# Kernel tuning notes

Measured on AMD Instinct MI355X. Metric: run time of the kernel, lower is better.

Reference implementation:

```python
import jax, jax.numpy as jnp
import numpy as np

B, L, D_MODEL = 2, 1024, 1024
N_LAYERS = 2
D_INNER = 2 * D_MODEL          # expand = 2
D_STATE = 16
D_CONV = 4
DT_RANK = (D_MODEL + 15) // 16  # ceil(d_model/16) = 64
INIT_SCALE = 0.02


def setup_inputs() -> dict:
    key = jax.random.key(0)
    ks = jax.random.split(key, 8)
    f32 = jnp.float32
    dt_init = float(np.log(np.expm1(0.01)))  # softplus^-1(0.01), standard mamba dt bias init
    return {
        "x": jax.random.normal(ks[0], (B, L, D_MODEL), f32),
        "W_in": jax.random.normal(ks[1], (N_LAYERS, 2 * D_INNER, D_MODEL), f32) * INIT_SCALE,
        "conv_w": jax.random.normal(ks[2], (N_LAYERS, D_INNER, D_CONV), f32) * INIT_SCALE,
        "conv_b": jnp.zeros((N_LAYERS, D_INNER), f32),
        "W_x": jax.random.normal(ks[3], (N_LAYERS, DT_RANK + 2 * D_STATE, D_INNER), f32) * INIT_SCALE,
        "W_dt": jax.random.normal(ks[4], (N_LAYERS, D_INNER, DT_RANK), f32) * INIT_SCALE,
        "b_dt": jnp.full((N_LAYERS, D_INNER), dt_init, f32),
        "A_log": jnp.tile(jnp.log(jnp.arange(1, D_STATE + 1, dtype=f32)), (N_LAYERS, D_INNER, 1)),
        "D": jnp.ones((N_LAYERS, D_INNER), f32),
        "W_out": jax.random.normal(ks[5], (N_LAYERS, D_MODEL, D_INNER), f32) * INIT_SCALE,
    }


def _silu(x):
    return x * jax.nn.sigmoid(x)


def _causal_conv1d(u, w, b):
    # u: [B, L, D_INNER], w: [D_INNER, D_CONV] depthwise, b: [D_INNER]
    ut = jnp.pad(jnp.transpose(u, (0, 2, 1)), ((0, 0), (0, 0), (D_CONV - 1, 0)))
    y = jax.lax.conv_general_dilated(
        ut, w[:, None, :], window_strides=(1,), padding='VALID',
        feature_group_count=D_INNER, dimension_numbers=('NCH', 'OIH', 'NCH'))
    return jnp.transpose(y + b[None, :, None], (0, 2, 1))


def _selective_scan(u, dt, A, Bm, Cm, Dvec):
    # u, dt: [B, L, D_INNER]; A: [D_INNER, N]; Bm, Cm: [B, L, N]; Dvec: [D_INNER]
    dA = jnp.exp(dt[..., None] * A)                        # [B,L,Din,N]
    dBu = dt[..., None] * Bm[:, :, None, :] * u[..., None]  # [B,L,Din,N]

    def step(h, xs):
        dA_t, dBu_t, C_t = xs                              # [B,Din,N],[B,Din,N],[B,N]
        h = dA_t * h + dBu_t
        y = jnp.einsum('bdn,bn->bd', h, C_t)
        return h, y

    h0 = jnp.zeros((u.shape[0], D_INNER, D_STATE), u.dtype)
    _, ys = jax.lax.scan(step, h0, (jnp.swapaxes(dA, 0, 1),
                                    jnp.swapaxes(dBu, 0, 1),
                                    jnp.swapaxes(Cm, 0, 1)))
    return jnp.swapaxes(ys, 0, 1) + u * Dvec               # [B,L,Din]


def _mamba_layer(x, W_in, conv_w, conv_b, W_x, W_dt, b_dt, A_log, Dvec, W_out):
    xz = jnp.einsum('bld,ed->ble', x, W_in)                # [B,L,2*Din]
    u, z = jnp.split(xz, 2, axis=-1)
    u = _silu(_causal_conv1d(u, conv_w, conv_b))
    x_dbl = jnp.einsum('bld,rd->blr', u, W_x)              # [B,L,dt_rank+2N]
    dt, Bm, Cm = jnp.split(x_dbl, [DT_RANK, DT_RANK + D_STATE], axis=-1)
    dt = jax.nn.softplus(jnp.einsum('blr,dr->bld', dt, W_dt) + b_dt)
    A = -jnp.exp(A_log)
    y = _selective_scan(u, dt, A, Bm, Cm, Dvec)
    y = y * _silu(z)
    return jnp.einsum('bld,od->blo', y, W_out)


def reference(x, W_in, conv_w, conv_b, W_x, W_dt, b_dt, A_log, D, W_out):
    residual = x
    h = x
    for i in range(N_LAYERS):
        h = _mamba_layer(h, W_in[i], conv_w[i], conv_b[i], W_x[i],
                         W_dt[i], b_dt[i], A_log[i], D[i], W_out[i])
    return h + residual
```

## Files before the change

### kernel.cpp

```cpp
#include <hip/hip_runtime.h>
#include <hip/hip_bf16.h>
#include <math.h>

#define B_ 2
#define L_ 1024
#define DM 1024
#define DIN 2048
#define DS 16
#define DTR 64
#define CHL 32
#define NCH 32

typedef __attribute__((ext_vector_type(8))) short bf16x8;
typedef __attribute__((ext_vector_type(8))) unsigned short u16x8;
typedef __attribute__((ext_vector_type(4))) unsigned short u16x4;
typedef __attribute__((ext_vector_type(4))) float f32x4;
typedef unsigned short ushort_t;
typedef unsigned int uint_t;

__device__ __forceinline__ float sigmoidf_(float x) { return 1.f / (1.f + __expf(-x)); }
__device__ __forceinline__ ushort_t f2b(float f) {
    uint_t b = __float_as_uint(f);
    return (ushort_t)((b + 0x7FFFu + ((b >> 16) & 1u)) >> 16);
}
__device__ __forceinline__ float b2f(ushort_t u) {
    return __uint_as_float(((uint_t)u) << 16);
}

__global__ __launch_bounds__(256) void f2b_all_k(
    const float* __restrict__ s0, ushort_t* __restrict__ d0, int n0,
    const float* __restrict__ s1, ushort_t* __restrict__ d1, int n1,
    const float* __restrict__ s2, ushort_t* __restrict__ d2, int n2,
    const float* __restrict__ s3, ushort_t* __restrict__ d3, int n3,
    const float* __restrict__ s4, ushort_t* __restrict__ d4, int n4)
{
    int i = (blockIdx.x * 256 + threadIdx.x) * 4;
    const float* s; ushort_t* d;
    if (i < n0) { s = s0; d = d0; }
    else { i -= n0;
    if (i < n1) { s = s1; d = d1; }
    else { i -= n1;
    if (i < n2) { s = s2; d = d2; }
    else { i -= n2;
    if (i < n3) { s = s3; d = d3; }
    else { i -= n3;
    if (i < n4) { s = s4; d = d4; }
    else return; }}}}
    float4 v = *(const float4*)(s + i);
    u16x4 o;
    o[0] = f2b(v.x); o[1] = f2b(v.y); o[2] = f2b(v.z); o[3] = f2b(v.w);
    *(u16x4*)(d + i) = o;
}

__device__ __forceinline__ int xcd_swz(int wgid, int nwg) {
    int cpx = nwg >> 3;
    return (wgid & 7) * cpx + (wgid >> 3);
}

__global__ __launch_bounds__(512) void mgemm_w(const ushort_t* __restrict__ A,
    const ushort_t* __restrict__ Bt, ushort_t* __restrict__ Cb,
    int M, int N, int K, int lda, int ldb)
{
    __shared__ ushort_t sA[2][128 * 32];
    __shared__ ushort_t sB[2][256 * 32];
    const int tid = threadIdx.x;
    const int lane = tid & 63, wv = tid >> 6;
    const int wm = wv >> 2, wn = wv & 3;
    const int swz = xcd_swz(blockIdx.y * gridDim.x + blockIdx.x, gridDim.x * gridDim.y);
    const int m0 = (swz / gridDim.x) * 128, n0 = (swz % gridDim.x) * 256;
    const int sr = tid >> 2;
    const int sc = (tid & 3) * 8;
    f32x4 acc[4][4] = {};

    __builtin_amdgcn_global_load_lds(
        (const uint_t*)(A + (size_t)(m0 + sr) * lda + sc),
        (uint_t*)(sA[0] + sr * 32 + sc), 16, 0, 0);
#pragma unroll
    for (int it = 0; it < 2; ++it) {
        int rb = (tid + it * 512) >> 2;
        __builtin_amdgcn_global_load_lds(
            (const uint_t*)(Bt + (size_t)(n0 + rb) * ldb + sc),
            (uint_t*)(sB[0] + rb * 32 + sc), 16, 0, 0);
    }
    __syncthreads();
    int cur = 0;
    for (int k0 = 0; k0 < K; k0 += 32) {
        if (k0 + 32 < K) {
            int nxt = cur ^ 1;
            __builtin_amdgcn_global_load_lds(
                (const uint_t*)(A + (size_t)(m0 + sr) * lda + k0 + 32 + sc),
                (uint_t*)(sA[nxt] + sr * 32 + sc), 16, 0, 0);
#pragma unroll
            for (int it = 0; it < 2; ++it) {
                int rb = (tid + it * 512) >> 2;
                __builtin_amdgcn_global_load_lds(
                    (const uint_t*)(Bt + (size_t)(n0 + rb) * ldb + k0 + 32 + sc),
                    (uint_t*)(sB[nxt] + rb * 32 + sc), 16, 0, 0);
            }
        }
        bf16x8 af[4], bfr[4];
#pragma unroll
        for (int i = 0; i < 4; ++i) {
            af[i]  = *(const bf16x8*)(sA[cur] + (wm * 64 + i * 16 + (lane & 15)) * 32 + (lane >> 4) * 8);
            bfr[i] = *(const bf16x8*)(sB[cur] + (wn * 64 + i * 16 + (lane & 15)) * 32 + (lane >> 4) * 8);
        }
#pragma unroll
        for (int i = 0; i < 4; ++i)
#pragma unroll
            for (int jj = 0; jj < 4; ++jj)
                acc[i][jj] = __builtin_amdgcn_mfma_f32_16x16x32_bf16(af[i], bfr[jj], acc[i][jj], 0, 0, 0);
        __syncthreads();
        cur ^= 1;
    }

    const int cr = (lane >> 4) * 4, cc = lane & 15;
#pragma unroll
    for (int i = 0; i < 4; ++i) {
        int mrow = m0 + wm * 64 + i * 16 + cr;
#pragma unroll
        for (int jj = 0; jj < 4; ++jj) {
            int ncol = n0 + wn * 64 + jj * 16 + cc;
#pragma unroll
            for (int r = 0; r < 4; ++r)
                Cb[(size_t)(mrow + r) * N + ncol] = f2b(acc[i][jj][r]);
        }
    }
}

__global__ __launch_bounds__(256) void mgemm_dt(const ushort_t* __restrict__ A,
    const ushort_t* __restrict__ Bt, ushort_t* __restrict__ Cb,
    const float* __restrict__ bias, int M, int N, int K, int lda, int ldb)
{
    __shared__ ushort_t sA[2][128 * 32];
    __shared__ ushort_t sB[2][128 * 32];
    const int tid = threadIdx.x;
    const int lane = tid & 63, wv = tid >> 6;
    const int wm = wv >> 1, wn = wv & 1;
    const int swz = xcd_swz(blockIdx.y * gridDim.x + blockIdx.x, gridDim.x * gridDim.y);
    const int m0 = (swz / gridDim.x) * 128, n0 = (swz % gridDim.x) * 128;
    const int sr = tid >> 2;
    const int sc = (tid & 3) * 8;
    f32x4 acc[4][4] = {};

#pragma unroll
    for (int j = 0; j < 2; ++j) {
        int ra = sr + j * 64;
        __builtin_amdgcn_global_load_lds(
            (const uint_t*)(A + (size_t)(m0 + ra) * lda + sc),
            (uint_t*)(sA[0] + ra * 32 + sc), 16, 0, 0);
        int gb = n0 + ra; if (gb >= N) gb = N - 1;
        __builtin_amdgcn_global_load_lds(
            (const uint_t*)(Bt + (size_t)gb * ldb + sc),
            (uint_t*)(sB[0] + ra * 32 + sc), 16, 0, 0);
    }
    __syncthreads();
    int cur = 0;
    for (int k0 = 0; k0 < K; k0 += 32) {
        if (k0 + 32 < K) {
            int nxt = cur ^ 1;
#pragma unroll
            for (int j = 0; j < 2; ++j) {
                int ra = sr + j * 64;
                __builtin_amdgcn_global_load_lds(
                    (const uint_t*)(A + (size_t)(m0 + ra) * lda + k0 + 32 + sc),
                    (uint_t*)(sA[nxt] + ra * 32 + sc), 16, 0, 0);
                int gb = n0 + ra; if (gb >= N) gb = N - 1;
                __builtin_amdgcn_global_load_lds(
                    (const uint_t*)(Bt + (size_t)gb * ldb + k0 + 32 + sc),
                    (uint_t*)(sB[nxt] + ra * 32 + sc), 16, 0, 0);
            }
        }
        bf16x8 af[4], bfr[4];
#pragma unroll
        for (int i = 0; i < 4; ++i) {
            af[i]  = *(const bf16x8*)(sA[cur] + (wm * 64 + i * 16 + (lane & 15)) * 32 + (lane >> 4) * 8);
            bfr[i] = *(const bf16x8*)(sB[cur] + (wn * 64 + i * 16 + (lane & 15)) * 32 + (lane >> 4) * 8);
        }
#pragma unroll
        for (int i = 0; i < 4; ++i)
#pragma unroll
            for (int jj = 0; jj < 4; ++jj)
                acc[i][jj] = __builtin_amdgcn_mfma_f32_16x16x32_bf16(af[i], bfr[jj], acc[i][jj], 0, 0, 0);
        __syncthreads();
        cur ^= 1;
    }

    const int cr = (lane >> 4) * 4, cc = lane & 15;
#pragma unroll
    for (int i = 0; i < 4; ++i) {
        int mrow = m0 + wm * 64 + i * 16 + cr;
#pragma unroll
        for (int jj = 0; jj < 4; ++jj) {
            int ncol = n0 + wn * 64 + jj * 16 + cc;
            if (ncol < N) {
#pragma unroll
                for (int r = 0; r < 4; ++r) {
                    float v = acc[i][jj][r];
                    size_t off = (size_t)(mrow + r) * N + ncol;
                    float s = v + bias[ncol];
                    Cb[off] = f2b((s > 20.f) ? s : log1pf(expf(s)));
                }
            }
        }
    }
}

__global__ __launch_bounds__(256) void mgemm_sk(const ushort_t* __restrict__ A,
    const ushort_t* __restrict__ Bt, float* __restrict__ P,
    int M, int N, int Kslice, int lda, int ldb)
{
    __shared__ ushort_t sA[2][128 * 32];
    __shared__ ushort_t sB[2][128 * 32];
    const int tid = threadIdx.x;
    const int lane = tid & 63, wv = tid >> 6;
    const int wm = wv >> 1, wn = wv & 1;
    const int m0 = blockIdx.y * 128;
    const int kbase = blockIdx.z * Kslice;
    const int sr = tid >> 2;
    const int sc = (tid & 3) * 8;
    f32x4 acc[4][4] = {};

#pragma unroll
    for (int j = 0; j < 2; ++j) {
        int ra = sr + j * 64;
        __builtin_amdgcn_global_load_lds(
            (const uint_t*)(A + (size_t)(m0 + ra) * lda + kbase + sc),
            (uint_t*)(sA[0] + ra * 32 + sc), 16, 0, 0);
        int gb = ra; if (gb >= N) gb = N - 1;
        __builtin_amdgcn_global_load_lds(
            (const uint_t*)(Bt + (size_t)gb * ldb + kbase + sc),
            (uint_t*)(sB[0] + ra * 32 + sc), 16, 0, 0);
    }
    __syncthreads();
    int cur = 0;
    for (int k0 = kbase; k0 < kbase + Kslice; k0 += 32) {
        if (k0 + 32 < kbase + Kslice) {
            int nxt = cur ^ 1;
#pragma unroll
            for (int j = 0; j < 2; ++j) {
                int ra = sr + j * 64;
                __builtin_amdgcn_global_load_lds(
                    (const uint_t*)(A + (size_t)(m0 + ra) * lda + k0 + 32 + sc),
                    (uint_t*)(sA[nxt] + ra * 32 + sc), 16, 0, 0);
                int gb = ra; if (gb >= N) gb = N - 1;
                __builtin_amdgcn_global_load_lds(
                    (const uint_t*)(Bt + (size_t)gb * ldb + k0 + 32 + sc),
                    (uint_t*)(sB[nxt] + ra * 32 + sc), 16, 0, 0);
            }
        }
        bf16x8 af[4], bfr[4];
#pragma unroll
        for (int i = 0; i < 4; ++i) {
            af[i]  = *(const bf16x8*)(sA[cur] + (wm * 64 + i * 16 + (lane & 15)) * 32 + (lane >> 4) * 8);
            bfr[i] = *(const bf16x8*)(sB[cur] + (wn * 64 + i * 16 + (lane & 15)) * 32 + (lane >> 4) * 8);
        }
#pragma unroll
        for (int i = 0; i < 4; ++i)
#pragma unroll
            for (int jj = 0; jj < 4; ++jj)
                acc[i][jj] = __builtin_amdgcn_mfma_f32_16x16x32_bf16(af[i], bfr[jj], acc[i][jj], 0, 0, 0);
        __syncthreads();
        cur ^= 1;
    }

    const int cr = (lane >> 4) * 4, cc = lane & 15;
    float* Pz = P + (size_t)blockIdx.z * M * 96;
#pragma unroll
    for (int i = 0; i < 4; ++i) {
        int mrow = m0 + wm * 64 + i * 16 + cr;
#pragma unroll
        for (int jj = 0; jj < 4; ++jj) {
            int ncol = wn * 64 + jj * 16 + cc;
            if (ncol < 96) {
#pragma unroll
                for (int r = 0; r < 4; ++r)
                    Pz[(size_t)(mrow + r) * 96 + ncol] = acc[i][jj][r];
            }
        }
    }
}

__global__ __launch_bounds__(256) void wxred_k(const float* __restrict__ P,
    float* __restrict__ xdbl, ushort_t* __restrict__ xdblb)
{
    int idx = blockIdx.x * 256 + threadIdx.x;
    float s = 0.f;
#pragma unroll
    for (int z = 0; z < 8; ++z) s += P[(size_t)z * 196608 + idx];
    xdbl[idx] = s;
    xdblb[idx] = f2b(s);
}

template<int EPI>
__global__ __launch_bounds__(256) void mgemm_n64(const ushort_t* __restrict__ A,
    const ushort_t* __restrict__ Bt, float* __restrict__ Cf, ushort_t* __restrict__ Cb,
    const float* __restrict__ res, int M, int N, int K, int lda, int ldb)
{
    __shared__ ushort_t sA[2][128 * 32];
    __shared__ ushort_t sB[2][64 * 32];
    const int tid = threadIdx.x;
    const int lane = tid & 63, wv = tid >> 6;
    const int swz = xcd_swz(blockIdx.y * gridDim.x + blockIdx.x, gridDim.x * gridDim.y);
    const int m0 = (swz / gridDim.x) * 128, n0 = (swz % gridDim.x) * 64;
    const int sr = tid >> 2;
    const int sc = (tid & 3) * 8;
    f32x4 acc[2][4] = {};

#pragma unroll
    for (int j = 0; j < 2; ++j) {
        int ra = sr + j * 64;
        __builtin_amdgcn_global_load_lds(
            (const uint_t*)(A + (size_t)(m0 + ra) * lda + sc),
            (uint_t*)(sA[0] + ra * 32 + sc), 16, 0, 0);
    }
    __builtin_amdgcn_global_load_lds(
        (const uint_t*)(Bt + (size_t)(n0 + sr) * ldb + sc),
        (uint_t*)(sB[0] + sr * 32 + sc), 16, 0, 0);
    __syncthreads();
    int cur = 0;
    for (int k0 = 0; k0 < K; k0 += 32) {
        if (k0 + 32 < K) {
            int nxt = cur ^ 1;
#pragma unroll
            for (int j = 0; j < 2; ++j) {
                int ra = sr + j * 64;
                __builtin_amdgcn_global_load_lds(
                    (const uint_t*)(A + (size_t)(m0 + ra) * lda + k0 + 32 + sc),
                    (uint_t*)(sA[nxt] + ra * 32 + sc), 16, 0, 0);
            }
            __builtin_amdgcn_global_load_lds(
                (const uint_t*)(Bt + (size_t)(n0 + sr) * ldb + k0 + 32 + sc),
                (uint_t*)(sB[nxt] + sr * 32 + sc), 16, 0, 0);
        }
        bf16x8 af[2], bfr[4];
#pragma unroll
        for (int i = 0; i < 2; ++i)
            af[i]  = *(const bf16x8*)(sA[cur] + (wv * 32 + i * 16 + (lane & 15)) * 32 + (lane >> 4) * 8);
#pragma unroll
        for (int jj = 0; jj < 4; ++jj)
            bfr[jj] = *(const bf16x8*)(sB[cur] + (jj * 16 + (lane & 15)) * 32 + (lane >> 4) * 8);
#pragma unroll
        for (int i = 0; i < 2; ++i)
#pragma unroll
            for (int jj = 0; jj < 4; ++jj)
                acc[i][jj] = __builtin_amdgcn_mfma_f32_16x16x32_bf16(af[i], bfr[jj], acc[i][jj], 0, 0, 0);
        __syncthreads();
        cur ^= 1;
    }

    const int cr = (lane >> 4) * 4, cc = lane & 15;
#pragma unroll
    for (int i = 0; i < 2; ++i) {
        int mrow = m0 + wv * 32 + i * 16 + cr;
#pragma unroll
        for (int jj = 0; jj < 4; ++jj) {
            int ncol = n0 + jj * 16 + cc;
#pragma unroll
            for (int r = 0; r < 4; ++r) {
                float v = acc[i][jj][r];
                size_t off = (size_t)(mrow + r) * N + ncol;
                if (EPI == 3) Cb[off] = f2b(v);
                else Cf[off] = v + res[off];
            }
        }
    }
}

__global__ __launch_bounds__(256) void conv8_k(const ushort_t* __restrict__ xzb,
    const float* __restrict__ cw, const float* __restrict__ cb,
    ushort_t* __restrict__ ucb)
{
    int idx8 = blockIdx.x * 256 + threadIdx.x;
    int d8 = (idx8 & 255) * 8;
    int t = (idx8 >> 8) & (L_ - 1);
    int b = idx8 >> 18;
    const ushort_t* base = xzb + (size_t)b * L_ * (2 * DIN) + d8;
    float acc[8];
    const float4* cb4 = (const float4*)(cb + d8);
    float4 cbl = cb4[0], cbh = cb4[1];
#pragma unroll
    for (int e = 0; e < 4; ++e) { acc[e] = ((const float*)&cbl)[e]; acc[4 + e] = ((const float*)&cbh)[e]; }
    float4 cwv[8];
#pragma unroll
    for (int e = 0; e < 8; ++e) cwv[e] = ((const float4*)cw)[d8 + e];
#pragma unroll
    for (int j = 0; j < 4; ++j) {
        int tt = t - 3 + j;
        if (tt >= 0) {
            u16x8 row = *(const u16x8*)(base + (size_t)tt * (2 * DIN));
#pragma unroll
            for (int e = 0; e < 8; ++e)
                acc[e] = fmaf(((const float*)&cwv[e])[j], b2f(row[e]), acc[e]);
        }
    }
    u16x8 ob;
#pragma unroll
    for (int e = 0; e < 8; ++e) {
        float v = acc[e] * sigmoidf_(acc[e]);
        ob[e] = f2b(v);
    }
    *(u16x8*)(ucb + (size_t)idx8 * 8) = ob;
}

__global__ __launch_bounds__(256, 2) void scan_s1(const ushort_t* __restrict__ dtfb,
    const ushort_t* __restrict__ ucb, const float* __restrict__ xdbl,
    const float* __restrict__ A_log,
    float* __restrict__ bnd_q, float* __restrict__ bnd_s)
{
    __shared__ uint_t sdt[CHL * 256];
    __shared__ float sB[CHL * 16];
    const int tid = threadIdx.x;
    const int bx = blockIdx.x;
    const int dg = bx & 7, c = (bx >> 3) & 31, b = bx >> 8;
    const int d = dg * 256 + tid;
    const int row0 = b * L_ + c * CHL;

    float A_dn[16];
#pragma unroll
    for (int n = 0; n < 16; ++n) A_dn[n] = -__expf(A_log[(size_t)d * DS + n]);

    for (int k = 0; k < CHL; ++k) {
        size_t off = (size_t)(row0 + k) * DIN + d;
        sdt[k * 256 + tid] = (uint_t)dtfb[off] | ((uint_t)ucb[off] << 16);
    }
#pragma unroll
    for (int j = 0; j < 2; ++j) {
        int idx = tid + j * 256;
        int t = idx >> 4, n = idx & 15;
        sB[idx] = xdbl[(size_t)(row0 + t) * 96 + 64 + n];
    }
    __syncthreads();

    float q[16];
#pragma unroll
    for (int n = 0; n < 16; ++n) q[n] = 0.f;
    float s = 0.f;
    for (int k = 0; k < CHL; ++k) {
        uint_t pk = sdt[k * 256 + tid];
        float dtv = __uint_as_float(pk << 16);
        float uv  = __uint_as_float(pk & 0xffff0000u);
        float dtu = dtv * uv;
        s += dtv;
        f32x4 Bq[4];
#pragma unroll
        for (int j = 0; j < 4; ++j) Bq[j] = *(const f32x4*)(sB + k * 16 + j * 4);
#pragma unroll
        for (int n = 0; n < 16; ++n)
            q[n] = fmaf(__expf(dtv * A_dn[n]), q[n], dtu * Bq[n >> 2][n & 3]);
    }
    float* qp = bnd_q + ((size_t)(b * NCH + c) * DIN + d) * 16;
#pragma unroll
    for (int j = 0; j < 4; ++j)
        *(f32x4*)(qp + j * 4) = (f32x4){q[j * 4], q[j * 4 + 1], q[j * 4 + 2], q[j * 4 + 3]};
    bnd_s[(size_t)(b * NCH + c) * DIN + d] = s;
}

__global__ __launch_bounds__(256, 2) void scan_s2(const ushort_t* __restrict__ dtfb,
    const ushort_t* __restrict__ ucb_in, const float* __restrict__ xdbl,
    const ushort_t* __restrict__ xzb, const float* __restrict__ A_log,
    const float* __restrict__ Dvec, const float* __restrict__ bnd_q,
    const float* __restrict__ bnd_s, ushort_t* __restrict__ ucb_out)
{
    __shared__ uint_t sdt[CHL * 256];
    __shared__ float sBC[CHL * 32];
    const int tid = threadIdx.x;
    const int bx = blockIdx.x;
    const int dg = bx & 7, c = (bx >> 3) & 31, b = bx >> 8;
    const int d = dg * 256 + tid;
    const int row0 = b * L_ + c * CHL;
    const float Dd = Dvec[d];

    float A_dn[16];
#pragma unroll
    for (int n = 0; n < 16; ++n) A_dn[n] = -__expf(A_log[(size_t)d * DS + n]);

    for (int k = 0; k < CHL; ++k) {
        size_t off = (size_t)(row0 + k) * DIN + d;
        sdt[k * 256 + tid] = (uint_t)dtfb[off] | ((uint_t)ucb_in[off] << 16);
    }
#pragma unroll
    for (int j = 0; j < 4; ++j) {
        int idx = tid + j * 256;
        int t = idx >> 5, jj = idx & 31;
        sBC[idx] = xdbl[(size_t)(row0 + t) * 96 + 64 + (jj & 1) * 16 + (jj >> 1)];
    }

    float h[16];
#pragma unroll
    for (int n = 0; n < 16; ++n) h[n] = 0.f;
    const size_t cb_base = (size_t)b * NCH * DIN + d;
    for (int cc = 0; cc < c; ++cc) {
        size_t idx = cb_base + (size_t)cc * DIN;
        float sv = bnd_s[idx];
        const float* qp = bnd_q + idx * 16;
        f32x4 qv[4];
#pragma unroll
        for (int j = 0; j < 4; ++j) qv[j] = *(const f32x4*)(qp + j * 4);
#pragma unroll
        for (int n = 0; n < 16; ++n)
            h[n] = fmaf(__expf(A_dn[n] * sv), h[n], qv[n >> 2][n & 3]);
    }
    __syncthreads();

    for (int k = 0; k < CHL; ++k) {
        uint_t pk = sdt[k * 256 + tid];
        float dtv = __uint_as_float(pk << 16);
        float uv  = __uint_as_float(pk & 0xffff0000u);
        float dtu = dtv * uv;
        float z = b2f(xzb[(size_t)(row0 + k) * (2 * DIN) + DIN + d]);
        float y = uv * Dd;
        f32x4 bcq[8];
#pragma unroll
        for (int j = 0; j < 8; ++j) bcq[j] = *(const f32x4*)(sBC + k * 32 + j * 4);
#pragma unroll
        for (int n = 0; n < 16; ++n) {
            float Bv = bcq[n >> 1][(n & 1) * 2];
            float Cv = bcq[n >> 1][(n & 1) * 2 + 1];
            h[n] = fmaf(__expf(dtv * A_dn[n]), h[n], dtu * Bv);
            y = fmaf(h[n], Cv, y);
        }
        y *= z * sigmoidf_(z);
        ucb_out[(size_t)(row0 + k) * DIN + d] = f2b(y);
    }
}

extern "C" void kernel_launch(void* const* d_in, const int* in_sizes, int n_in,
                              void* d_out, int out_size, void* d_ws, size_t ws_size,
                              hipStream_t stream)
{
    (void)in_sizes; (void)n_in; (void)out_size; (void)ws_size;
    const float* x      = (const float*)d_in[0];
    const float* W_in   = (const float*)d_in[1];
    const float* conv_w = (const float*)d_in[2];
    const float* conv_b = (const float*)d_in[3];
    const float* W_x    = (const float*)d_in[4];
    const float* W_dt   = (const float*)d_in[5];
    const float* b_dt   = (const float*)d_in[6];
    const float* A_log  = (const float*)d_in[7];
    const float* Dv     = (const float*)d_in[8];
    const float* W_out  = (const float*)d_in[9];
    float* out = (float*)d_out;

    float* xdbl    = (float*)d_ws;
    float* pws     = xdbl + 196608;
    float* bnd_q   = pws + 1572864;
    float* bnd_s   = bnd_q + 2097152;
    ushort_t* dtfb = (ushort_t*)(bnd_s + 131072);
    ushort_t* xzb  = dtfb + 4194304;
    ushort_t* ucb  = xzb + 8388608;
    ushort_t* xdblb= ucb + 4194304;
    ushort_t* xb   = xdblb + 196608;
    ushort_t* wib  = xb + 2097152;
    ushort_t* wxb  = wib + 8388608;
    ushort_t* wdb  = wxb + 393216;
    ushort_t* wob  = wdb + 262144;

    const int M = B_ * L_;
    const int NT = 2097152 + 8388608 + 393216 + 262144 + 4194304;
    f2b_all_k<<<(NT / 4) / 256, 256, 0, stream>>>(
        x, xb, 2097152, W_in, wib, 8388608, W_x, wxb, 393216,
        W_dt, wdb, 262144, W_out, wob, 4194304);

    for (int layer = 0; layer < 2; ++layer) {
        mgemm_w<<<dim3(4096 / 256, M / 128), 512, 0, stream>>>(
            xb, wib + (size_t)layer * 4194304, xzb, M, 2 * DIN, DM, DM, DM);
        conv8_k<<<(B_ * L_ * DIN / 8) / 256, 256, 0, stream>>>(
            xzb, conv_w + (size_t)layer * DIN * 4, conv_b + (size_t)layer * DIN, ucb);
        mgemm_sk<<<dim3(1, M / 128, 8), 256, 0, stream>>>(
            ucb, wxb + (size_t)layer * 196608, pws, M, 96, DIN / 8, DIN, DIN);
        wxred_k<<<196608 / 256, 256, 0, stream>>>(pws, xdbl, xdblb);
        mgemm_dt<<<dim3(2048 / 128, M / 128), 256, 0, stream>>>(
            xdblb, wdb + (size_t)layer * 131072, dtfb,
            b_dt + (size_t)layer * DIN, M, DIN, DTR, 96, DTR);
        const float* Al = A_log + (size_t)layer * DIN * DS;
        scan_s1<<<B_ * NCH * 8, 256, 0, stream>>>(dtfb, ucb, xdbl, Al, bnd_q, bnd_s);
        scan_s2<<<B_ * NCH * 8, 256, 0, stream>>>(dtfb, ucb, xdbl, xzb, Al,
            Dv + (size_t)layer * DIN, bnd_q, bnd_s, ucb);
        if (layer == 0)
            mgemm_n64<3><<<dim3(1024 / 64, M / 128), 256, 0, stream>>>(
                ucb, wob + (size_t)layer * 2097152, nullptr, xb, nullptr,
                M, DM, DIN, DIN, DIN);
        else
            mgemm_n64<4><<<dim3(1024 / 64, M / 128), 256, 0, stream>>>(
                ucb, wob + (size_t)layer * 2097152, out, nullptr, x,
                M, DM, DIN, DIN, DIN);
    }
}
```

Before: 456.8 us.

## Fuse split-K reduction into dt projection GEMM and retile input GEMM

Removes the separate split-K reduction kernel by having the dt-projection GEMM sum the eight partial slices directly into shared memory as bf16, with block column 0 also writing the B/C columns of xdbl in fp32. The input projection GEMM switches from a 512-thread 128x256 tile to a 256-thread 128x128 tile, doubling the grid. This saves one launch and a round trip of the reduced x_dbl buffer, but every block now re-reads and re-sums the same partial slices, adding redundant global reads.

```diff
diff --git a/kernel.cpp b/kernel.cpp
--- a/kernel.cpp
+++ b/kernel.cpp
@@ -57,79 +57,9 @@
     return (wgid & 7) * cpx + (wgid >> 3);
 }
 
-__global__ __launch_bounds__(512) void mgemm_w(const ushort_t* __restrict__ A,
+__global__ __launch_bounds__(256) void mgemm_in(const ushort_t* __restrict__ A,
     const ushort_t* __restrict__ Bt, ushort_t* __restrict__ Cb,
     int M, int N, int K, int lda, int ldb)
-{
-    __shared__ ushort_t sA[2][128 * 32];
-    __shared__ ushort_t sB[2][256 * 32];
-    const int tid = threadIdx.x;
-    const int lane = tid & 63, wv = tid >> 6;
-    const int wm = wv >> 2, wn = wv & 3;
-    const int swz = xcd_swz(blockIdx.y * gridDim.x + blockIdx.x, gridDim.x * gridDim.y);
-    const int m0 = (swz / gridDim.x) * 128, n0 = (swz % gridDim.x) * 256;
-    const int sr = tid >> 2;
-    const int sc = (tid & 3) * 8;
-    f32x4 acc[4][4] = {};
-
-    __builtin_amdgcn_global_load_lds(
-        (const uint_t*)(A + (size_t)(m0 + sr) * lda + sc),
-        (uint_t*)(sA[0] + sr * 32 + sc), 16, 0, 0);
-#pragma unroll
-    for (int it = 0; it < 2; ++it) {
-        int rb = (tid + it * 512) >> 2;
-        __builtin_amdgcn_global_load_lds(
-            (const uint_t*)(Bt + (size_t)(n0 + rb) * ldb + sc),
-            (uint_t*)(sB[0] + rb * 32 + sc), 16, 0, 0);
-    }
-    __syncthreads();
-    int cur = 0;
-    for (int k0 = 0; k0 < K; k0 += 32) {
-        if (k0 + 32 < K) {
-            int nxt = cur ^ 1;
-            __builtin_amdgcn_global_load_lds(
-                (const uint_t*)(A + (size_t)(m0 + sr) * lda + k0 + 32 + sc),
-                (uint_t*)(sA[nxt] + sr * 32 + sc), 16, 0, 0);
-#pragma unroll
-            for (int it = 0; it < 2; ++it) {
-                int rb = (tid + it * 512) >> 2;
-                __builtin_amdgcn_global_load_lds(
-                    (const uint_t*)(Bt + (size_t)(n0 + rb) * ldb + k0 + 32 + sc),
-                    (uint_t*)(sB[nxt] + rb * 32 + sc), 16, 0, 0);
-            }
-        }
-        bf16x8 af[4], bfr[4];
-#pragma unroll
-        for (int i = 0; i < 4; ++i) {
-            af[i]  = *(const bf16x8*)(sA[cur] + (wm * 64 + i * 16 + (lane & 15)) * 32 + (lane >> 4) * 8);
-            bfr[i] = *(const bf16x8*)(sB[cur] + (wn * 64 + i * 16 + (lane & 15)) * 32 + (lane >> 4) * 8);
-        }
-#pragma unroll
-        for (int i = 0; i < 4; ++i)
-#pragma unroll
-            for (int jj = 0; jj < 4; ++jj)
-                acc[i][jj] = __builtin_amdgcn_mfma_f32_16x16x32_bf16(af[i], bfr[jj], acc[i][jj], 0, 0, 0);
-        __syncthreads();
-        cur ^= 1;
-    }
-
-    const int cr = (lane >> 4) * 4, cc = lane & 15;
-#pragma unroll
-    for (int i = 0; i < 4; ++i) {
-        int mrow = m0 + wm * 64 + i * 16 + cr;
-#pragma unroll
-        for (int jj = 0; jj < 4; ++jj) {
-            int ncol = n0 + wn * 64 + jj * 16 + cc;
-#pragma unroll
-            for (int r = 0; r < 4; ++r)
-                Cb[(size_t)(mrow + r) * N + ncol] = f2b(acc[i][jj][r]);
-        }
-    }
-}
-
-__global__ __launch_bounds__(256) void mgemm_dt(const ushort_t* __restrict__ A,
-    const ushort_t* __restrict__ Bt, ushort_t* __restrict__ Cb,
-    const float* __restrict__ bias, int M, int N, int K, int lda, int ldb)
 {
     __shared__ ushort_t sA[2][128 * 32];
     __shared__ ushort_t sB[2][128 * 32];
@@ -148,9 +78,8 @@
         __builtin_amdgcn_global_load_lds(
             (const uint_t*)(A + (size_t)(m0 + ra) * lda + sc),
             (uint_t*)(sA[0] + ra * 32 + sc), 16, 0, 0);
-        int gb = n0 + ra; if (gb >= N) gb = N - 1;
         __builtin_amdgcn_global_load_lds(
-            (const uint_t*)(Bt + (size_t)gb * ldb + sc),
+            (const uint_t*)(Bt + (size_t)(n0 + ra) * ldb + sc),
             (uint_t*)(sB[0] + ra * 32 + sc), 16, 0, 0);
     }
     __syncthreads();
@@ -164,9 +93,8 @@
                 __builtin_amdgcn_global_load_lds(
                     (const uint_t*)(A + (size_t)(m0 + ra) * lda + k0 + 32 + sc),
                     (uint_t*)(sA[nxt] + ra * 32 + sc), 16, 0, 0);
-                int gb = n0 + ra; if (gb >= N) gb = N - 1;
                 __builtin_amdgcn_global_load_lds(
-                    (const uint_t*)(Bt + (size_t)gb * ldb + k0 + 32 + sc),
+                    (const uint_t*)(Bt + (size_t)(n0 + ra) * ldb + k0 + 32 + sc),
                     (uint_t*)(sB[nxt] + ra * 32 + sc), 16, 0, 0);
             }
         }
@@ -192,15 +120,9 @@
 #pragma unroll
         for (int jj = 0; jj < 4; ++jj) {
             int ncol = n0 + wn * 64 + jj * 16 + cc;
-            if (ncol < N) {
-#pragma unroll
-                for (int r = 0; r < 4; ++r) {
-                    float v = acc[i][jj][r];
-                    size_t off = (size_t)(mrow + r) * N + ncol;
-                    float s = v + bias[ncol];
-                    Cb[off] = f2b((s > 20.f) ? s : log1pf(expf(s)));
-                }
-            }
+#pragma unroll
+            for (int r = 0; r < 4; ++r)
+                Cb[(size_t)(mrow + r) * N + ncol] = f2b(acc[i][jj][r]);
         }
     }
 }
@@ -280,15 +202,89 @@
     }
 }
 
-__global__ __launch_bounds__(256) void wxred_k(const float* __restrict__ P,
-    float* __restrict__ xdbl, ushort_t* __restrict__ xdblb)
-{
-    int idx = blockIdx.x * 256 + threadIdx.x;
-    float s = 0.f;
-#pragma unroll
-    for (int z = 0; z < 8; ++z) s += P[(size_t)z * 196608 + idx];
-    xdbl[idx] = s;
-    xdblb[idx] = f2b(s);
+__global__ __launch_bounds__(256) void mgemm_dtf(const float* __restrict__ P,
+    const ushort_t* __restrict__ Wd, const float* __restrict__ bias,
+    float* __restrict__ xdbl, ushort_t* __restrict__ dtfb)
+{
+    __shared__ ushort_t sA[2][128 * 36];
+    __shared__ ushort_t sB[2][128 * 32];
+    const int tid = threadIdx.x;
+    const int lane = tid & 63, wv = tid >> 6;
+    const int wm = wv >> 1, wn = wv & 1;
+    const int n0 = blockIdx.x * 128, m0 = blockIdx.y * 128;
+
+#pragma unroll
+    for (int kh = 0; kh < 2; ++kh)
+#pragma unroll
+        for (int it = 0; it < 2; ++it) {
+            int ci = tid + it * 256;
+            int row = ci >> 2, cc = ci & 3;
+            __builtin_amdgcn_global_load_lds(
+                (const uint_t*)(Wd + (size_t)(n0 + row) * 64 + kh * 32 + cc * 8),
+                (uint_t*)(sB[kh] + (size_t)ci * 8), 16, 0, 0);
+        }
+
+#pragma unroll
+    for (int it = 0; it < 8; ++it) {
+        int ci = tid + it * 256;
+        int row = ci >> 4, c4 = (ci & 15) * 4;
+        float s0 = 0.f, s1 = 0.f, s2 = 0.f, s3 = 0.f;
+#pragma unroll
+        for (int z = 0; z < 8; ++z) {
+            f32x4 v = *(const f32x4*)(P + (size_t)z * 196608 + (size_t)(m0 + row) * 96 + c4);
+            s0 += v[0]; s1 += v[1]; s2 += v[2]; s3 += v[3];
+        }
+        u16x4 o; o[0] = f2b(s0); o[1] = f2b(s1); o[2] = f2b(s2); o[3] = f2b(s3);
+        int kh = c4 >> 5, cl = c4 & 31;
+        *(u16x4*)(sA[kh] + row * 36 + cl) = o;
+    }
+    if (blockIdx.x == 0) {
+#pragma unroll
+        for (int it = 0; it < 4; ++it) {
+            int ci = tid + it * 256;
+            int row = ci >> 3, c4 = (ci & 7) * 4;
+            f32x4 s = {0.f, 0.f, 0.f, 0.f};
+#pragma unroll
+            for (int z = 0; z < 8; ++z) {
+                f32x4 v = *(const f32x4*)(P + (size_t)z * 196608 + (size_t)(m0 + row) * 96 + 64 + c4);
+                s[0] += v[0]; s[1] += v[1]; s[2] += v[2]; s[3] += v[3];
+            }
+            *(f32x4*)(xdbl + (size_t)(m0 + row) * 96 + 64 + c4) = s;
+        }
+    }
+    __syncthreads();
+
+    f32x4 acc[4][4] = {};
+#pragma unroll
+    for (int ks = 0; ks < 2; ++ks) {
+        bf16x8 af[4], bfr[4];
+#pragma unroll
+        for (int i = 0; i < 4; ++i) {
+            af[i]  = *(const bf16x8*)(sA[ks] + (wm * 64 + i * 16 + (lane & 15)) * 36 + (lane >> 4) * 8);
+            bfr[i] = *(const bf16x8*)(sB[ks] + (wn * 64 + i * 16 + (lane & 15)) * 32 + (lane >> 4) * 8);
+        }
+#pragma unroll
+        for (int i = 0; i < 4; ++i)
+#pragma unroll
+            for (int jj = 0; jj < 4; ++jj)
+                acc[i][jj] = __builtin_amdgcn_mfma_f32_16x16x32_bf16(af[i], bfr[jj], acc[i][jj], 0, 0, 0);
+    }
+
+    const int cr = (lane >> 4) * 4, cc = lane & 15;
+#pragma unroll
+    for (int i = 0; i < 4; ++i) {
+        int mrow = m0 + wm * 64 + i * 16 + cr;
+#pragma unroll
+        for (int jj = 0; jj < 4; ++jj) {
+            int ncol = n0 + wn * 64 + jj * 16 + cc;
+#pragma unroll
+            for (int r = 0; r < 4; ++r) {
+                float s = acc[i][jj][r] + bias[ncol];
+                dtfb[(size_t)(mrow + r) * DIN + ncol] =
+                    f2b((s > 20.f) ? s : log1pf(expf(s)));
+            }
+        }
+    }
 }
 
 template<int EPI>
@@ -548,8 +544,7 @@
     ushort_t* dtfb = (ushort_t*)(bnd_s + 131072);
     ushort_t* xzb  = dtfb + 4194304;
     ushort_t* ucb  = xzb + 8388608;
-    ushort_t* xdblb= ucb + 4194304;
-    ushort_t* xb   = xdblb + 196608;
+    ushort_t* xb   = ucb + 4194304;
     ushort_t* wib  = xb + 2097152;
     ushort_t* wxb  = wib + 8388608;
     ushort_t* wdb  = wxb + 393216;
@@ -562,16 +557,14 @@
         W_dt, wdb, 262144, W_out, wob, 4194304);
 
     for (int layer = 0; layer < 2; ++layer) {
-        mgemm_w<<<dim3(4096 / 256, M / 128), 512, 0, stream>>>(
+        mgemm_in<<<dim3(4096 / 128, M / 128), 256, 0, stream>>>(
             xb, wib + (size_t)layer * 4194304, xzb, M, 2 * DIN, DM, DM, DM);
         conv8_k<<<(B_ * L_ * DIN / 8) / 256, 256, 0, stream>>>(
             xzb, conv_w + (size_t)layer * DIN * 4, conv_b + (size_t)layer * DIN, ucb);
         mgemm_sk<<<dim3(1, M / 128, 8), 256, 0, stream>>>(
             ucb, wxb + (size_t)layer * 196608, pws, M, 96, DIN / 8, DIN, DIN);
-        wxred_k<<<196608 / 256, 256, 0, stream>>>(pws, xdbl, xdblb);
-        mgemm_dt<<<dim3(2048 / 128, M / 128), 256, 0, stream>>>(
-            xdblb, wdb + (size_t)layer * 131072, dtfb,
-            b_dt + (size_t)layer * DIN, M, DIN, DTR, 96, DTR);
+        mgemm_dtf<<<dim3(16, 16), 256, 0, stream>>>(
+            pws, wdb + (size_t)layer * 131072, b_dt + (size_t)layer * DIN, xdbl, dtfb);
         const float* Al = A_log + (size_t)layer * DIN * DS;
         scan_s1<<<B_ * NCH * 8, 256, 0, stream>>>(dtfb, ucb, xdbl, Al, bnd_q, bnd_s);
         scan_s2<<<B_ * NCH * 8, 256, 0, stream>>>(dtfb, ucb, xdbl, xzb, Al,
```

Result: no change. 451.1 us (-1.2%).
